# Kernel tuning notes

Measured on AMD Instinct MI355X. Metric: run time of the kernel, lower is better.

Reference implementation:

```python
import jax, jax.numpy as jnp
import numpy as np

N_NODES = 100000
N_EDGES = 600000
D_IN = 128
D_OUT = 512  # hidden_size * gates_num = 128 * 4


def setup_inputs() -> dict:
    key = jax.random.key(0)
    k1, k2, k3, k4 = jax.random.split(key, 4)
    x = jax.random.normal(k1, (N_NODES, D_IN), dtype=jnp.float32)
    edge_index = jax.random.randint(k2, (2, N_EDGES), 0, N_NODES, dtype=jnp.int64)
    W = jax.random.normal(k3, (D_OUT, D_IN), dtype=jnp.float32) * (1.0 / np.sqrt(D_IN))
    b = jax.random.normal(k4, (D_OUT,), dtype=jnp.float32) * 0.01
    return {"x": x, "edge_index": edge_index, "W": W, "b": b}


def reference(x, edge_index, W, b):
    row, col = edge_index[0], edge_index[1]
    # gather neighbor features and scatter-add into destination nodes
    agg = jax.ops.segment_sum(x[col], row, num_segments=x.shape[0])  # [N, D_IN]
    out = x + agg  # residual
    return out @ W.T + b  # [N, D_OUT]
```

## Files before the change

kernel.cpp:

```cpp
#include <hip/hip_runtime.h>
#include <hip/hip_bf16.h>

#define N_NODES 100000
#define N_EDGES 600000
#define D_IN 128
#define D_OUT 512
#define CAP 40
#define OVF_CAP 1024

typedef __bf16 bf16x8 __attribute__((ext_vector_type(8)));
typedef __bf16 bf16x2 __attribute__((ext_vector_type(2)));
typedef float f32x4 __attribute__((ext_vector_type(4)));

#define OFF_CNT   25600000
#define OFF_OVFC  26000000
#define OFF_OVF   26000016
#define OFF_BUCK  26008208
#define OFF_XB    42008208
#define OFF_WB    67608208

__device__ inline bf16x8 cvt8(float4 v0, float4 v1) {
    bf16x8 u = { (__bf16)v0.x, (__bf16)v0.y, (__bf16)v0.z, (__bf16)v0.w,
                 (__bf16)v1.x, (__bf16)v1.y, (__bf16)v1.z, (__bf16)v1.w };
    return u;
}

__device__ inline float blo(unsigned int u) { return __uint_as_float(u << 16); }
__device__ inline float bhi(unsigned int u) { return __uint_as_float(u & 0xffff0000u); }

#define EB  2344
#define XB  6250
#define WBK 32
__global__ void k_bucket_cvt(const int* __restrict__ ei, const float* __restrict__ x,
                             const float* __restrict__ W, int* __restrict__ cnt,
                             int* __restrict__ bucket, int* __restrict__ ovf_cnt,
                             int2* __restrict__ ovf, __bf16* __restrict__ xb,
                             __bf16* __restrict__ wb) {
    int b = blockIdx.x;
    if (b < EB) {
        int e = b * 256 + threadIdx.x;
        if (e >= N_EDGES) return;
        int r = ei[e];
        int c = ei[N_EDGES + e];
        int slot = atomicAdd(&cnt[r], 1);
        if (slot < CAP) {
            bucket[(size_t)r * CAP + slot] = c;
        } else {
            int oi = atomicAdd(ovf_cnt, 1);
            if (oi < OVF_CAP) ovf[oi] = make_int2(r, c);
        }
    } else if (b < EB + XB) {
        size_t i = (size_t)(b - EB) * 2048 + threadIdx.x * 8;
        float4 v0 = *(const float4*)(x + i);
        float4 v1 = *(const float4*)(x + i + 4);
        *(bf16x8*)(xb + i) = cvt8(v0, v1);
    } else {
        size_t i = (size_t)(b - EB - XB) * 2048 + threadIdx.x * 8;
        float4 v0 = *(const float4*)(W + i);
        float4 v1 = *(const float4*)(W + i + 4);
        *(bf16x8*)(wb + i) = cvt8(v0, v1);
    }
}

__global__ void k_agg(const float* __restrict__ x, const __bf16* __restrict__ xb,
                      const int* __restrict__ cnt, const int* __restrict__ bucket,
                      const int* __restrict__ ovf_cnt, const int2* __restrict__ ovf,
                      __bf16* __restrict__ h) {
    int w = (blockIdx.x * blockDim.x + threadIdx.x) >> 6;
    if (w >= N_NODES / 2) return;
    int lane = threadIdx.x & 63;
    int gA = w * 2;
    int gB = gA + 1;
    const unsigned int* xbu = (const unsigned int*)xb;

    const int* bkA = bucket + (size_t)gA * CAP;
    const int* bkB = bucket + (size_t)gB * CAP;
    int mA = (lane < CAP) ? bkA[lane] : 0;
    int mB = (lane < CAP) ? bkB[lane] : 0;
    int2 c2 = ((const int2*)cnt)[w];
    unsigned int rA = xbu[(size_t)gA * 64 + lane];
    unsigned int rB = xbu[(size_t)gB * 64 + lane];

    int degA = __builtin_amdgcn_readfirstlane(c2.x);
    int degB = __builtin_amdgcn_readfirstlane(c2.y);
    int dA = degA < CAP ? degA : CAP;
    int dB = degB < CAP ? degB : CAP;
    int dmax = dA > dB ? dA : dB;

    float aX0 = blo(rA), aY0 = bhi(rA), aX1 = 0.f, aY1 = 0.f;
    float bX0 = blo(rB), bY0 = bhi(rB), bX1 = 0.f, bY1 = 0.f;

    for (int d = 0; d < dmax; d += 2) {
        int  cA0 = (d     < dA) ? __builtin_amdgcn_readlane(mA, d)     : 0;
        int  cA1 = (d + 1 < dA) ? __builtin_amdgcn_readlane(mA, d + 1) : 0;
        int  cB0 = (d     < dB) ? __builtin_amdgcn_readlane(mB, d)     : 0;
        int  cB1 = (d + 1 < dB) ? __builtin_amdgcn_readlane(mB, d + 1) : 0;
        float sA0 = (d     < dA) ? 1.f : 0.f;
        float sA1 = (d + 1 < dA) ? 1.f : 0.f;
        float sB0 = (d     < dB) ? 1.f : 0.f;
        float sB1 = (d + 1 < dB) ? 1.f : 0.f;
        unsigned int uA0 = xbu[(size_t)cA0 * 64 + lane];
        unsigned int uA1 = xbu[(size_t)cA1 * 64 + lane];
        unsigned int uB0 = xbu[(size_t)cB0 * 64 + lane];
        unsigned int uB1 = xbu[(size_t)cB1 * 64 + lane];
        aX0 = fmaf(sA0, blo(uA0), aX0); aY0 = fmaf(sA0, bhi(uA0), aY0);
        aX1 = fmaf(sA1, blo(uA1), aX1); aY1 = fmaf(sA1, bhi(uA1), aY1);
        bX0 = fmaf(sB0, blo(uB0), bX0); bY0 = fmaf(sB0, bhi(uB0), bY0);
        bX1 = fmaf(sB1, blo(uB1), bX1); bY1 = fmaf(sB1, bhi(uB1), bY1);
    }
    aX0 += aX1; aY0 += aY1;
    bX0 += bX1; bY0 += bY1;

    if (degA > CAP || degB > CAP) {
        const float2* xr = (const float2*)x;
        int n = *ovf_cnt;
        if (n > OVF_CAP) n = OVF_CAP;
        for (int i = 0; i < n; ++i) {
            int2 e = ovf[i];
            if (e.x == gA) {
                float2 v = xr[(size_t)e.y * 64 + lane];
                aX0 += v.x; aY0 += v.y;
            }
            if (e.x == gB) {
                float2 v = xr[(size_t)e.y * 64 + lane];
                bX0 += v.x; bY0 += v.y;
            }
        }
    }

    bf16x2 oA = { (__bf16)aX0, (__bf16)aY0 };
    bf16x2 oB = { (__bf16)bX0, (__bf16)bY0 };
    ((bf16x2*)h)[(size_t)gA * 64 + lane] = oA;
    ((bf16x2*)h)[(size_t)gB * 64 + lane] = oB;
}

#define BM 128
#define BN 128
#define LDA 136
#define LDB 136
#define NWG 3128

__launch_bounds__(512, 4)
__global__ void k_gemm(const __bf16* __restrict__ h, const __bf16* __restrict__ wb,
                       const float* __restrict__ bias, float* __restrict__ out) {
    __shared__ __bf16 As[BM * LDA];
    __shared__ __bf16 Bs[BN * LDB];

    int tid = threadIdx.x;

    int bid = blockIdx.x;
    int wg = (bid & 7) * (NWG / 8) + (bid >> 3);
    int m0 = (wg >> 2) * BM;
    int n0 = (wg & 3) * BN;

    #pragma unroll
    for (int it = 0; it < 4; ++it) {
        int i = tid + it * 512;
        int r = i >> 4;
        int c = (i & 15) << 3;
        int gr = m0 + r;
        if (gr > N_NODES - 1) gr = N_NODES - 1;
        *(bf16x8*)&As[r * LDA + c] = *(const bf16x8*)(h + (size_t)gr * D_IN + c);
    }
    #pragma unroll
    for (int it = 0; it < 4; ++it) {
        int i = tid + it * 512;
        int r = i >> 4;
        int c = (i & 15) << 3;
        *(bf16x8*)&Bs[r * LDB + c] = *(const bf16x8*)(wb + (size_t)(n0 + r) * D_IN + c);
    }
    __syncthreads();

    int lane = tid & 63;
    int wave = tid >> 6;
    int wm = wave & 1;
    int wn = wave >> 1;
    int quad = lane >> 4;
    int l16 = lane & 15;

    f32x4 acc[4][2] = {};

    const __bf16* Abase = &As[(wm * 64 + l16) * LDA + quad * 8];
    const __bf16* Bbase = &Bs[(wn * 32 + l16) * LDB + quad * 8];

    #pragma unroll
    for (int ks = 0; ks < 4; ++ks) {
        bf16x8 a0 = *(const bf16x8*)(Abase + ks * 32);
        bf16x8 a1 = *(const bf16x8*)(Abase + 16 * LDA + ks * 32);
        bf16x8 a2 = *(const bf16x8*)(Abase + 32 * LDA + ks * 32);
        bf16x8 a3 = *(const bf16x8*)(Abase + 48 * LDA + ks * 32);
        bf16x8 b0 = *(const bf16x8*)(Bbase + ks * 32);
        bf16x8 b1 = *(const bf16x8*)(Bbase + 16 * LDB + ks * 32);
        acc[0][0] = __builtin_amdgcn_mfma_f32_16x16x32_bf16(a0, b0, acc[0][0], 0, 0, 0);
        acc[0][1] = __builtin_amdgcn_mfma_f32_16x16x32_bf16(a0, b1, acc[0][1], 0, 0, 0);
        acc[1][0] = __builtin_amdgcn_mfma_f32_16x16x32_bf16(a1, b0, acc[1][0], 0, 0, 0);
        acc[1][1] = __builtin_amdgcn_mfma_f32_16x16x32_bf16(a1, b1, acc[1][1], 0, 0, 0);
        acc[2][0] = __builtin_amdgcn_mfma_f32_16x16x32_bf16(a2, b0, acc[2][0], 0, 0, 0);
        acc[2][1] = __builtin_amdgcn_mfma_f32_16x16x32_bf16(a2, b1, acc[2][1], 0, 0, 0);
        acc[3][0] = __builtin_amdgcn_mfma_f32_16x16x32_bf16(a3, b0, acc[3][0], 0, 0, 0);
        acc[3][1] = __builtin_amdgcn_mfma_f32_16x16x32_bf16(a3, b1, acc[3][1], 0, 0, 0);
    }

    float bias0 = bias[n0 + wn * 32 + l16];
    float bias1 = bias[n0 + wn * 32 + 16 + l16];
    #pragma unroll
    for (int mt = 0; mt < 4; ++mt) {
        int mrow = m0 + wm * 64 + mt * 16 + quad * 4;
        #pragma unroll
        for (int nt = 0; nt < 2; ++nt) {
            int ncol = n0 + wn * 32 + nt * 16 + l16;
            float bv = nt ? bias1 : bias0;
            #pragma unroll
            for (int rg = 0; rg < 4; ++rg) {
                int m = mrow + rg;
                if (m < N_NODES)
                    __builtin_nontemporal_store(acc[mt][nt][rg] + bv,
                                                &out[(size_t)m * D_OUT + ncol]);
            }
        }
    }
}

extern "C" void kernel_launch(void* const* d_in, const int* in_sizes, int n_in,
                              void* d_out, int out_size, void* d_ws, size_t ws_size,
                              hipStream_t stream) {
    const float* x  = (const float*)d_in[0];
    const int*   ei = (const int*)d_in[1];
    const float* W  = (const float*)d_in[2];
    const float* b  = (const float*)d_in[3];
    float* out = (float*)d_out;

    char* ws = (char*)d_ws;
    __bf16* h    = (__bf16*)ws;
    int* cnt     = (int*)(ws + OFF_CNT);
    int* ovf_cnt = (int*)(ws + OFF_OVFC);
    int2* ovf    = (int2*)(ws + OFF_OVF);
    int* bucket  = (int*)(ws + OFF_BUCK);
    __bf16* xb   = (__bf16*)(ws + OFF_XB);
    __bf16* wb   = (__bf16*)(ws + OFF_WB);

    hipMemsetAsync(cnt, 0, (OFF_OVFC - OFF_CNT) + 16, stream);

    k_bucket_cvt<<<EB + XB + WBK, 256, 0, stream>>>(ei, x, W, cnt, bucket,
                                                    ovf_cnt, ovf, xb, wb);
    k_agg<<<(N_NODES / 2 * 64 + 255) / 256, 256, 0, stream>>>(x, xb, cnt, bucket,
                                                              ovf_cnt, ovf, h);
    k_gemm<<<NWG, 512, 0, stream>>>(h, wb, b, out);
}
```

Measured before the change: 351.7 us.

## Fuse neighbor aggregation into GEMM block, keeping aggregated tile in LDS

Merges the aggregation and GEMM kernels into one. Each 512-thread block aggregates 128 node rows straight into shared memory, prefetching bucket and count data for the next row pair and unrolling the gather by four. It then loops over the four 128-column output tiles, reloading W each time. This drops the intermediate h round trip through global memory and one launch. In exchange there are far fewer blocks (782), so the latency-bound gather has less parallelism, and the per-block serial phases may lower occupancy.

Result: no change. 352.9 us (+0.4%).

```diff
diff --git a/kernel.cpp b/kernel.cpp
--- a/kernel.cpp
+++ b/kernel.cpp
@@ -62,160 +62,179 @@
     }
 }
 
-__global__ void k_agg(const float* __restrict__ x, const __bf16* __restrict__ xb,
-                      const int* __restrict__ cnt, const int* __restrict__ bucket,
-                      const int* __restrict__ ovf_cnt, const int2* __restrict__ ovf,
-                      __bf16* __restrict__ h) {
-    int w = (blockIdx.x * blockDim.x + threadIdx.x) >> 6;
-    if (w >= N_NODES / 2) return;
-    int lane = threadIdx.x & 63;
-    int gA = w * 2;
-    int gB = gA + 1;
-    const unsigned int* xbu = (const unsigned int*)xb;
-
-    const int* bkA = bucket + (size_t)gA * CAP;
-    const int* bkB = bucket + (size_t)gB * CAP;
-    int mA = (lane < CAP) ? bkA[lane] : 0;
-    int mB = (lane < CAP) ? bkB[lane] : 0;
-    int2 c2 = ((const int2*)cnt)[w];
-    unsigned int rA = xbu[(size_t)gA * 64 + lane];
-    unsigned int rB = xbu[(size_t)gB * 64 + lane];
-
-    int degA = __builtin_amdgcn_readfirstlane(c2.x);
-    int degB = __builtin_amdgcn_readfirstlane(c2.y);
-    int dA = degA < CAP ? degA : CAP;
-    int dB = degB < CAP ? degB : CAP;
-    int dmax = dA > dB ? dA : dB;
-
-    float aX0 = blo(rA), aY0 = bhi(rA), aX1 = 0.f, aY1 = 0.f;
-    float bX0 = blo(rB), bY0 = bhi(rB), bX1 = 0.f, bY1 = 0.f;
-
-    for (int d = 0; d < dmax; d += 2) {
-        int  cA0 = (d     < dA) ? __builtin_amdgcn_readlane(mA, d)     : 0;
-        int  cA1 = (d + 1 < dA) ? __builtin_amdgcn_readlane(mA, d + 1) : 0;
-        int  cB0 = (d     < dB) ? __builtin_amdgcn_readlane(mB, d)     : 0;
-        int  cB1 = (d + 1 < dB) ? __builtin_amdgcn_readlane(mB, d + 1) : 0;
-        float sA0 = (d     < dA) ? 1.f : 0.f;
-        float sA1 = (d + 1 < dA) ? 1.f : 0.f;
-        float sB0 = (d     < dB) ? 1.f : 0.f;
-        float sB1 = (d + 1 < dB) ? 1.f : 0.f;
-        unsigned int uA0 = xbu[(size_t)cA0 * 64 + lane];
-        unsigned int uA1 = xbu[(size_t)cA1 * 64 + lane];
-        unsigned int uB0 = xbu[(size_t)cB0 * 64 + lane];
-        unsigned int uB1 = xbu[(size_t)cB1 * 64 + lane];
-        aX0 = fmaf(sA0, blo(uA0), aX0); aY0 = fmaf(sA0, bhi(uA0), aY0);
-        aX1 = fmaf(sA1, blo(uA1), aX1); aY1 = fmaf(sA1, bhi(uA1), aY1);
-        bX0 = fmaf(sB0, blo(uB0), bX0); bY0 = fmaf(sB0, bhi(uB0), bY0);
-        bX1 = fmaf(sB1, blo(uB1), bX1); bY1 = fmaf(sB1, bhi(uB1), bY1);
-    }
-    aX0 += aX1; aY0 += aY1;
-    bX0 += bX1; bY0 += bY1;
-
-    if (degA > CAP || degB > CAP) {
-        const float2* xr = (const float2*)x;
-        int n = *ovf_cnt;
-        if (n > OVF_CAP) n = OVF_CAP;
-        for (int i = 0; i < n; ++i) {
-            int2 e = ovf[i];
-            if (e.x == gA) {
-                float2 v = xr[(size_t)e.y * 64 + lane];
-                aX0 += v.x; aY0 += v.y;
-            }
-            if (e.x == gB) {
-                float2 v = xr[(size_t)e.y * 64 + lane];
-                bX0 += v.x; bY0 += v.y;
-            }
-        }
-    }
-
-    bf16x2 oA = { (__bf16)aX0, (__bf16)aY0 };
-    bf16x2 oB = { (__bf16)bX0, (__bf16)bY0 };
-    ((bf16x2*)h)[(size_t)gA * 64 + lane] = oA;
-    ((bf16x2*)h)[(size_t)gB * 64 + lane] = oB;
-}
-
 #define BM 128
-#define BN 128
 #define LDA 136
 #define LDB 136
-#define NWG 3128
+#define NBLK 782
 
 __launch_bounds__(512, 4)
-__global__ void k_gemm(const __bf16* __restrict__ h, const __bf16* __restrict__ wb,
-                       const float* __restrict__ bias, float* __restrict__ out) {
+__global__ void k_fused(const float* __restrict__ x, const __bf16* __restrict__ xb,
+                        const __bf16* __restrict__ wb, const int* __restrict__ cnt,
+                        const int* __restrict__ bucket, const int* __restrict__ ovf_cnt,
+                        const int2* __restrict__ ovf, const float* __restrict__ bias,
+                        float* __restrict__ out) {
     __shared__ __bf16 As[BM * LDA];
-    __shared__ __bf16 Bs[BN * LDB];
-
-    int tid = threadIdx.x;
-
-    int bid = blockIdx.x;
-    int wg = (bid & 7) * (NWG / 8) + (bid >> 3);
-    int m0 = (wg >> 2) * BM;
-    int n0 = (wg & 3) * BN;
+    __shared__ __bf16 Bs[128 * LDB];
+
+    int tid  = threadIdx.x;
+    int lane = tid & 63;
+    int wave = tid >> 6;
+    int m0   = blockIdx.x * BM;
+    const unsigned int* xbu = (const unsigned int*)xb;
+
+    auto loadp = [&](int p, int& mA, int& mB, unsigned int& rA, unsigned int& rB,
+                     int& cA, int& cB) {
+        int iA = p * 16 + wave * 2;
+        int gA = m0 + iA;     if (gA > N_NODES - 1) gA = N_NODES - 1;
+        int gB = m0 + iA + 1; if (gB > N_NODES - 1) gB = N_NODES - 1;
+        mA = (lane < CAP) ? bucket[(size_t)gA * CAP + lane] : 0;
+        mB = (lane < CAP) ? bucket[(size_t)gB * CAP + lane] : 0;
+        rA = xbu[(size_t)gA * 64 + lane];
+        rB = xbu[(size_t)gB * 64 + lane];
+        cA = cnt[gA];
+        cB = cnt[gB];
+    };
+
+    int pmA, pmB, pcA, pcB;
+    unsigned int prA, prB;
+    loadp(0, pmA, pmB, prA, prB, pcA, pcB);
 
     #pragma unroll
-    for (int it = 0; it < 4; ++it) {
-        int i = tid + it * 512;
-        int r = i >> 4;
-        int c = (i & 15) << 3;
-        int gr = m0 + r;
-        if (gr > N_NODES - 1) gr = N_NODES - 1;
-        *(bf16x8*)&As[r * LDA + c] = *(const bf16x8*)(h + (size_t)gr * D_IN + c);
-    }
-    #pragma unroll
-    for (int it = 0; it < 4; ++it) {
-        int i = tid + it * 512;
-        int r = i >> 4;
-        int c = (i & 15) << 3;
-        *(bf16x8*)&Bs[r * LDB + c] = *(const bf16x8*)(wb + (size_t)(n0 + r) * D_IN + c);
+    for (int p = 0; p < 8; ++p) {
+        int mA = pmA, mB = pmB, cA = pcA, cB = pcB;
+        unsigned int rA = prA, rB = prB;
+        if (p < 7) loadp(p + 1, pmA, pmB, prA, prB, pcA, pcB);
+
+        int iA = p * 16 + wave * 2;
+        int gA = m0 + iA;     if (gA > N_NODES - 1) gA = N_NODES - 1;
+        int gB = m0 + iA + 1; if (gB > N_NODES - 1) gB = N_NODES - 1;
+
+        int degA = __builtin_amdgcn_readfirstlane(cA);
+        int degB = __builtin_amdgcn_readfirstlane(cB);
+        int dA = degA < CAP ? degA : CAP;
+        int dB = degB < CAP ? degB : CAP;
+        int dmax = dA > dB ? dA : dB;
+
+        float aX0 = blo(rA), aY0 = bhi(rA), aX1 = 0.f, aY1 = 0.f;
+        float bX0 = blo(rB), bY0 = bhi(rB), bX1 = 0.f, bY1 = 0.f;
+
+        for (int d = 0; d < dmax; d += 4) {
+            int cA0 = (d     < dA) ? __builtin_amdgcn_readlane(mA, d)     : 0;
+            int cA1 = (d + 1 < dA) ? __builtin_amdgcn_readlane(mA, d + 1) : 0;
+            int cA2 = (d + 2 < dA) ? __builtin_amdgcn_readlane(mA, d + 2) : 0;
+            int cA3 = (d + 3 < dA) ? __builtin_amdgcn_readlane(mA, d + 3) : 0;
+            int cB0 = (d     < dB) ? __builtin_amdgcn_readlane(mB, d)     : 0;
+            int cB1 = (d + 1 < dB) ? __builtin_amdgcn_readlane(mB, d + 1) : 0;
+            int cB2 = (d + 2 < dB) ? __builtin_amdgcn_readlane(mB, d + 2) : 0;
+            int cB3 = (d + 3 < dB) ? __builtin_amdgcn_readlane(mB, d + 3) : 0;
+            float sA0 = (d     < dA) ? 1.f : 0.f;
+            float sA1 = (d + 1 < dA) ? 1.f : 0.f;
+            float sA2 = (d + 2 < dA) ? 1.f : 0.f;
+            float sA3 = (d + 3 < dA) ? 1.f : 0.f;
+            float sB0 = (d     < dB) ? 1.f : 0.f;
+            float sB1 = (d + 1 < dB) ? 1.f : 0.f;
+            float sB2 = (d + 2 < dB) ? 1.f : 0.f;
+            float sB3 = (d + 3 < dB) ? 1.f : 0.f;
+            unsigned int uA0 = xbu[(size_t)cA0 * 64 + lane];
+            unsigned int uA1 = xbu[(size_t)cA1 * 64 + lane];
+            unsigned int uA2 = xbu[(size_t)cA2 * 64 + lane];
+            unsigned int uA3 = xbu[(size_t)cA3 * 64 + lane];
+            unsigned int uB0 = xbu[(size_t)cB0 * 64 + lane];
+            unsigned int uB1 = xbu[(size_t)cB1 * 64 + lane];
+            unsigned int uB2 = xbu[(size_t)cB2 * 64 + lane];
+            unsigned int uB3 = xbu[(size_t)cB3 * 64 + lane];
+            aX0 = fmaf(sA0, blo(uA0), aX0); aY0 = fmaf(sA0, bhi(uA0), aY0);
+            aX1 = fmaf(sA1, blo(uA1), aX1); aY1 = fmaf(sA1, bhi(uA1), aY1);
+            aX0 = fmaf(sA2, blo(uA2), aX0); aY0 = fmaf(sA2, bhi(uA2), aY0);
+            aX1 = fmaf(sA3, blo(uA3), aX1); aY1 = fmaf(sA3, bhi(uA3), aY1);
+            bX0 = fmaf(sB0, blo(uB0), bX0); bY0 = fmaf(sB0, bhi(uB0), bY0);
+            bX1 = fmaf(sB1, blo(uB1), bX1); bY1 = fmaf(sB1, bhi(uB1), bY1);
+            bX0 = fmaf(sB2, blo(uB2), bX0); bY0 = fmaf(sB2, bhi(uB2), bY0);
+            bX1 = fmaf(sB3, blo(uB3), bX1); bY1 = fmaf(sB3, bhi(uB3), bY1);
+        }
+        aX0 += aX1; aY0 += aY1;
+        bX0 += bX1; bY0 += bY1;
+
+        if (degA > CAP || degB > CAP) {
+            const float2* xr = (const float2*)x;
+            int n = *ovf_cnt;
+            if (n > OVF_CAP) n = OVF_CAP;
+            for (int i = 0; i < n; ++i) {
+                int2 e = ovf[i];
+                if (e.x == gA) {
+                    float2 v = xr[(size_t)e.y * 64 + lane];
+                    aX0 += v.x; aY0 += v.y;
+                }
+                if (e.x == gB) {
+                    float2 v = xr[(size_t)e.y * 64 + lane];
+                    bX0 += v.x; bY0 += v.y;
+                }
+            }
+        }
+
+        bf16x2 oA = { (__bf16)aX0, (__bf16)aY0 };
+        bf16x2 oB = { (__bf16)bX0, (__bf16)bY0 };
+        *(bf16x2*)&As[iA * LDA + 2 * lane] = oA;
+        *(bf16x2*)&As[(iA + 1) * LDA + 2 * lane] = oB;
     }
     __syncthreads();
 
-    int lane = tid & 63;
-    int wave = tid >> 6;
     int wm = wave & 1;
     int wn = wave >> 1;
     int quad = lane >> 4;
     int l16 = lane & 15;
-
-    f32x4 acc[4][2] = {};
-
     const __bf16* Abase = &As[(wm * 64 + l16) * LDA + quad * 8];
     const __bf16* Bbase = &Bs[(wn * 32 + l16) * LDB + quad * 8];
 
-    #pragma unroll
-    for (int ks = 0; ks < 4; ++ks) {
-        bf16x8 a0 = *(const bf16x8*)(Abase + ks * 32);
-        bf16x8 a1 = *(const bf16x8*)(Abase + 16 * LDA + ks * 32);
-        bf16x8 a2 = *(const bf16x8*)(Abase + 32 * LDA + ks * 32);
-        bf16x8 a3 = *(const bf16x8*)(Abase + 48 * LDA + ks * 32);
-        bf16x8 b0 = *(const bf16x8*)(Bbase + ks * 32);
-        bf16x8 b1 = *(const bf16x8*)(Bbase + 16 * LDB + ks * 32);
-        acc[0][0] = __builtin_amdgcn_mfma_f32_16x16x32_bf16(a0, b0, acc[0][0], 0, 0, 0);
-        acc[0][1] = __builtin_amdgcn_mfma_f32_16x16x32_bf16(a0, b1, acc[0][1], 0, 0, 0);
-        acc[1][0] = __builtin_amdgcn_mfma_f32_16x16x32_bf16(a1, b0, acc[1][0], 0, 0, 0);
-        acc[1][1] = __builtin_amdgcn_mfma_f32_16x16x32_bf16(a1, b1, acc[1][1], 0, 0, 0);
-        acc[2][0] = __builtin_amdgcn_mfma_f32_16x16x32_bf16(a2, b0, acc[2][0], 0, 0, 0);
-        acc[2][1] = __builtin_amdgcn_mfma_f32_16x16x32_bf16(a2, b1, acc[2][1], 0, 0, 0);
-        acc[3][0] = __builtin_amdgcn_mfma_f32_16x16x32_bf16(a3, b0, acc[3][0], 0, 0, 0);
-        acc[3][1] = __builtin_amdgcn_mfma_f32_16x16x32_bf16(a3, b1, acc[3][1], 0, 0, 0);
-    }
-
-    float bias0 = bias[n0 + wn * 32 + l16];
-    float bias1 = bias[n0 + wn * 32 + 16 + l16];
-    #pragma unroll
-    for (int mt = 0; mt < 4; ++mt) {
-        int mrow = m0 + wm * 64 + mt * 16 + quad * 4;
+    #pragma unroll 1
+    for (int nq = 0; nq < 4; ++nq) {
+        if (nq) __syncthreads();
+        int n0 = nq * 128;
         #pragma unroll
-        for (int nt = 0; nt < 2; ++nt) {
-            int ncol = n0 + wn * 32 + nt * 16 + l16;
-            float bv = nt ? bias1 : bias0;
+        for (int it = 0; it < 4; ++it) {
+            int i = tid + it * 512;
+            int r = i >> 4;
+            int c = (i & 15) << 3;
+            *(bf16x8*)&Bs[r * LDB + c] =
+                *(const bf16x8*)(wb + (size_t)(n0 + r) * D_IN + c);
+        }
+        __syncthreads();
+
+        f32x4 acc[4][2] = {};
+        #pragma unroll
+        for (int ks = 0; ks < 4; ++ks) {
+            bf16x8 a0 = *(const bf16x8*)(Abase + ks * 32);
+            bf16x8 a1 = *(const bf16x8*)(Abase + 16 * LDA + ks * 32);
+            bf16x8 a2 = *(const bf16x8*)(Abase + 32 * LDA + ks * 32);
+            bf16x8 a3 = *(const bf16x8*)(Abase + 48 * LDA + ks * 32);
+            bf16x8 b0 = *(const bf16x8*)(Bbase + ks * 32);
+            bf16x8 b1 = *(const bf16x8*)(Bbase + 16 * LDB + ks * 32);
+            acc[0][0] = __builtin_amdgcn_mfma_f32_16x16x32_bf16(a0, b0, acc[0][0], 0, 0, 0);
+            acc[0][1] = __builtin_amdgcn_mfma_f32_16x16x32_bf16(a0, b1, acc[0][1], 0, 0, 0);
+            acc[1][0] = __builtin_amdgcn_mfma_f32_16x16x32_bf16(a1, b0, acc[1][0], 0, 0, 0);
+            acc[1][1] = __builtin_amdgcn_mfma_f32_16x16x32_bf16(a1, b1, acc[1][1], 0, 0, 0);
+            acc[2][0] = __builtin_amdgcn_mfma_f32_16x16x32_bf16(a2, b0, acc[2][0], 0, 0, 0);
+            acc[2][1] = __builtin_amdgcn_mfma_f32_16x16x32_bf16(a2, b1, acc[2][1], 0, 0, 0);
+            acc[3][0] = __builtin_amdgcn_mfma_f32_16x16x32_bf16(a3, b0, acc[3][0], 0, 0, 0);
+            acc[3][1] = __builtin_amdgcn_mfma_f32_16x16x32_bf16(a3, b1, acc[3][1], 0, 0, 0);
+        }
+
+        float bias0 = bias[n0 + wn * 32 + l16];
+        float bias1 = bias[n0 + wn * 32 + 16 + l16];
+        #pragma unroll
+        for (int mt = 0; mt < 4; ++mt) {
+            int mrow = m0 + wm * 64 + mt * 16 + quad * 4;
             #pragma unroll
-            for (int rg = 0; rg < 4; ++rg) {
-                int m = mrow + rg;
-                if (m < N_NODES)
-                    __builtin_nontemporal_store(acc[mt][nt][rg] + bv,
-                                                &out[(size_t)m * D_OUT + ncol]);
+            for (int nt = 0; nt < 2; ++nt) {
+                int ncol = n0 + wn * 32 + nt * 16 + l16;
+                float bv = nt ? bias1 : bias0;
+                #pragma unroll
+                for (int rg = 0; rg < 4; ++rg) {
+                    int m = mrow + rg;
+                    if (m < N_NODES)
+                        __builtin_nontemporal_store(acc[mt][nt][rg] + bv,
+                                                    &out[(size_t)m * D_OUT + ncol]);
+                }
             }
         }
     }
@@ -231,7 +250,6 @@
     float* out = (float*)d_out;
 
     char* ws = (char*)d_ws;
-    __bf16* h    = (__bf16*)ws;
     int* cnt     = (int*)(ws + OFF_CNT);
     int* ovf_cnt = (int*)(ws + OFF_OVFC);
     int2* ovf    = (int2*)(ws + OFF_OVF);
@@ -243,7 +261,5 @@
 
     k_bucket_cvt<<<EB + XB + WBK, 256, 0, stream>>>(ei, x, W, cnt, bucket,
                                                     ovf_cnt, ovf, xb, wb);
-    k_agg<<<(N_NODES / 2 * 64 + 255) / 256, 256, 0, stream>>>(x, xb, cnt, bucket,
-                                                              ovf_cnt, ovf, h);
-    k_gemm<<<NWG, 512, 0, stream>>>(h, wb, b, out);
-}
+    k_fused<<<NBLK, 512, 0, stream>>>(x, xb, wb, cnt, bucket, ovf_cnt, ovf, b, out);
+}
```
